# Kernel tuning notes

Hardware: AMD Instinct MI355X
Metric: run time of the kernel (lower is better)

Reference implementation:

```python
import jax, jax.numpy as jnp
import numpy as np

B, L, BERT_DIM = 8, 1024, 1024
HEADS, HEAD_SIZE = 12, 64


def setup_inputs() -> dict:
    key = jax.random.key(0)
    k1, k2, k3, k4, k5, k6 = jax.random.split(key, 6)
    s = 1.0 / np.sqrt(BERT_DIM)
    return {
        "head": jax.random.normal(k1, (B, L, BERT_DIM), dtype=jnp.float32),
        "tail": jax.random.normal(k2, (B, L, BERT_DIM), dtype=jnp.float32),
        "W_head": jax.random.normal(k3, (BERT_DIM, HEADS * HEAD_SIZE), dtype=jnp.float32) * s,
        "b_head": jax.random.normal(k4, (HEADS * HEAD_SIZE,), dtype=jnp.float32) * 0.01,
        "W_tail": jax.random.normal(k5, (BERT_DIM, HEADS * HEAD_SIZE), dtype=jnp.float32) * s,
        "b_tail": jax.random.normal(k6, (HEADS * HEAD_SIZE,), dtype=jnp.float32) * 0.01,
    }


def _sincos(seq_len, dim, dtype):
    # SinusoidalPositionEmbedding with merge_mode='zero': (L, dim), interleaved [sin, cos]
    pos = jnp.arange(seq_len, dtype=dtype)                     # (L,)
    inv = jnp.power(10000.0, -2.0 * jnp.arange(dim // 2, dtype=dtype) / dim)  # (dim/2,)
    ang = pos[:, None] * inv[None, :]                          # (L, dim/2)
    emb = jnp.stack([jnp.sin(ang), jnp.cos(ang)], axis=-1).reshape(seq_len, dim)
    # cos_pos: even/odd duplication as in torch reference
    cos_pos = jnp.repeat(emb[:, 1::2], 2, axis=-1)             # (L, dim)
    sin_pos = jnp.repeat(emb[:, 0::2], 2, axis=-1)             # (L, dim)
    return cos_pos, sin_pos


def _rotate_half(x):
    # stack([-x[...,1::2], x[...,::2]], -1).reshape(x.shape)
    return jnp.stack([-x[..., 1::2], x[..., 0::2]], axis=-1).reshape(x.shape)


def reference(head, tail, W_head, b_head, W_tail, b_tail):
    bsz, seq_len, _ = head.shape
    h = (head @ W_head + b_head).reshape(bsz, seq_len, HEADS, HEAD_SIZE)
    t = (tail @ W_tail + b_tail).reshape(bsz, seq_len, HEADS, HEAD_SIZE)

    cos_pos, sin_pos = _sincos(seq_len, HEAD_SIZE, h.dtype)
    cos_pos = cos_pos[None, :, None, :]  # (1, L, 1, D)
    sin_pos = sin_pos[None, :, None, :]

    h = h * cos_pos + _rotate_half(h) * sin_pos
    t = t * cos_pos + _rotate_half(t) * sin_pos

    # (B, H, L, L)
    logits = jnp.einsum("blhd,bmhd->bhlm", h, t)
    return logits / jnp.sqrt(jnp.asarray(HEAD_SIZE, h.dtype))
```

## Files before the change

### kernel.cpp

```cpp
#include <hip/hip_runtime.h>
#include <hip/hip_bf16.h>


#define DIM   1024
#define NOUT  768
#define NHEAD 12

typedef __attribute__((ext_vector_type(8))) short bf16x8;
typedef __attribute__((ext_vector_type(4))) float f32x4;

__device__ __forceinline__ ushort f2bf(float f) {
  union { float f; unsigned u; } v; v.f = f;
  unsigned r = v.u + 0x7fffu + ((v.u >> 16) & 1u);
  return (ushort)(r >> 16);
}

__device__ __forceinline__ void gload16(const ushort* g, ushort* l) {
  __builtin_amdgcn_global_load_lds(
      (const __attribute__((address_space(1))) unsigned int*)g,
      (__attribute__((address_space(3))) unsigned int*)l, 16, 0, 0);
}

__global__ __launch_bounds__(256) void prep_kernel(
    const float* __restrict__ head, const float* __restrict__ tail,
    const float* __restrict__ Wh,   const float* __restrict__ Wt_,
    ushort* __restrict__ Hx, ushort* __restrict__ Tx,
    ushort* __restrict__ WtH, ushort* __restrict__ WtT,
    float2* __restrict__ rope)
{
  __shared__ ushort lds[64][72];
  const int bx = blockIdx.x, tid = threadIdx.x;

  if (bx < 4096) {
    size_t t = (size_t)bx * 256 + tid;
    const float* src; ushort* dst; size_t e;
    if (t < 524288) { src = head; dst = Hx; e = t * 16; }
    else            { src = tail; dst = Tx; e = (t - 524288) * 16; }
    const float4* p = reinterpret_cast<const float4*>(src + e);
    float4 a = p[0], b = p[1], c = p[2], d = p[3];
    ushort o[16] = { f2bf(a.x), f2bf(a.y), f2bf(a.z), f2bf(a.w),
                     f2bf(b.x), f2bf(b.y), f2bf(b.z), f2bf(b.w),
                     f2bf(c.x), f2bf(c.y), f2bf(c.z), f2bf(c.w),
                     f2bf(d.x), f2bf(d.y), f2bf(d.z), f2bf(d.w) };
    *reinterpret_cast<bf16x8*>(dst + e)     = *reinterpret_cast<bf16x8*>(o);
    *reinterpret_cast<bf16x8*>(dst + e + 8) = *reinterpret_cast<bf16x8*>(o + 8);
  } else if (bx < 4480) {
    int t2 = bx - 4096;
    int wsel = t2 / 192, tile = t2 % 192;
    int k0 = (tile / 12) * 64, n0 = (tile % 12) * 64;
    const float* W = wsel ? Wt_ : Wh;
    ushort* WT = wsel ? WtT : WtH;
#pragma unroll
    for (int q = 0; q < 16; ++q) {
      int idx = q * 256 + tid;
      int kr = idx >> 6, nc = idx & 63;
      lds[nc][kr] = f2bf(W[(size_t)(k0 + kr) * NOUT + n0 + nc]);
    }
    __syncthreads();
#pragma unroll
    for (int q = 0; q < 2; ++q) {
      int idx = q * 256 + tid;
      int nc = idx >> 3, kg = idx & 7;
      *reinterpret_cast<bf16x8*>(&WT[(size_t)(n0 + nc) * DIM + k0 + kg * 8]) =
          *reinterpret_cast<bf16x8*>(&lds[nc][kg * 8]);
    }
  } else {
    int j = (bx - 4480) * 256 + tid;
    int l = j >> 5, i = j & 31;
    float inv = powf(10000.0f, -(float)i / 32.0f);
    float ang = (float)l * inv;
    rope[j] = make_float2(cosf(ang), sinf(ang));
  }
}

__global__ __launch_bounds__(256) void proj_rope_kernel(
    const ushort* __restrict__ Hx,  const ushort* __restrict__ Tx,
    const ushort* __restrict__ WtH, const ushort* __restrict__ WtT,
    const float*  __restrict__ bh,  const float*  __restrict__ bt,
    const float2* __restrict__ rope,
    ushort* __restrict__ Hb, ushort* __restrict__ Tb)
{
  const bool sel = (blockIdx.z != 0);
  const ushort* X    = sel ? Tx  : Hx;
  const ushort* Wt   = sel ? WtT : WtH;
  const float*  bias = sel ? bt  : bh;
  ushort*       Out  = sel ? Tb  : Hb;

  __shared__ ushort As[128 * 64];
  __shared__ ushort Bs[128 * 64];

  const int tid = threadIdx.x;
  const int m0 = blockIdx.x * 128;
  const int n0 = blockIdx.y * 128;
  const int wid = tid >> 6, lane = tid & 63;
  const int wm = wid >> 1, wn = wid & 1;
  const int r = lane & 15, g = lane >> 4;
  const int r7 = r & 7;

  f32x4 acc[4][4] = {};

  for (int k0 = 0; k0 < DIM; k0 += 64) {
#pragma unroll
    for (int i = 0; i < 4; ++i) {
      int task = i * 256 + tid;
      int row = task >> 3, c = task & 7;
      int csrc = c ^ (row & 7);
      gload16(X + (size_t)(m0 + row) * DIM + k0 + csrc * 8, &As[task * 8]);
    }
#pragma unroll
    for (int i = 0; i < 4; ++i) {
      int task = i * 256 + tid;
      int row = task >> 3, c = task & 7;
      int csrc = c ^ (row & 7);
      gload16(Wt + (size_t)(n0 + row) * DIM + k0 + csrc * 8, &Bs[task * 8]);
    }
    __syncthreads();

    bf16x8 af[2][4], bfv[2][4];
#pragma unroll
    for (int ks = 0; ks < 2; ++ks) {
      int cs = (ks * 4 + g) ^ r7;
#pragma unroll
      for (int m = 0; m < 4; ++m)
        af[ks][m] = *reinterpret_cast<const bf16x8*>(
            &As[(wm * 64 + m * 16 + r) * 64 + cs * 8]);
#pragma unroll
      for (int n = 0; n < 4; ++n)
        bfv[ks][n] = *reinterpret_cast<const bf16x8*>(
            &Bs[(wn * 64 + n * 16 + r) * 64 + cs * 8]);
    }
#pragma unroll
    for (int n = 0; n < 4; ++n)
#pragma unroll
      for (int m = 0; m < 4; ++m) {
        acc[n][m] = __builtin_amdgcn_mfma_f32_16x16x32_bf16(
            bfv[0][n], af[0][m], acc[n][m], 0, 0, 0);
        acc[n][m] = __builtin_amdgcn_mfma_f32_16x16x32_bf16(
            bfv[1][n], af[1][m], acc[n][m], 0, 0, 0);
      }
    __syncthreads();
  }

#pragma unroll
  for (int n = 0; n < 4; ++n) {
    int col = n0 + wn * 64 + n * 16 + g * 4;
    int hd = col >> 6, dd = col & 63;
    int ii = dd >> 1;
    float4 bs4 = *reinterpret_cast<const float4*>(&bias[col]);
#pragma unroll
    for (int m = 0; m < 4; ++m) {
      int grow = m0 + wm * 64 + m * 16 + r;
      int l = grow & 1023, b = grow >> 10;
      float4 rp = *reinterpret_cast<const float4*>(&rope[l * 32 + ii]);
      float v0 = acc[n][m][0] + bs4.x;
      float v1 = acc[n][m][1] + bs4.y;
      float v2 = acc[n][m][2] + bs4.z;
      float v3 = acc[n][m][3] + bs4.w;
      ushort o[4] = { f2bf(v0 * rp.x - v1 * rp.y),
                      f2bf(v1 * rp.x + v0 * rp.y),
                      f2bf(v2 * rp.z - v3 * rp.w),
                      f2bf(v3 * rp.z + v2 * rp.w) };
      *reinterpret_cast<ushort4*>(
          &Out[(((size_t)b * NHEAD + hd) * 1024 + l) * 64 + dd]) =
          *reinterpret_cast<ushort4*>(o);
    }
  }
}

__global__ __launch_bounds__(256) void logits_kernel(
    const ushort* __restrict__ Hb, const ushort* __restrict__ Tb,
    float* __restrict__ out)
{
  const int f = blockIdx.x;
  const int rx = f & 7, q = f >> 3;
  const int j = q & 63, zq = q >> 6;
  const int z = zq * 8 + rx;
  const int l0 = (j & 7) * 128, m0 = (j >> 3) * 128;

  const int tid = threadIdx.x;
  const int wid = tid >> 6, lane = tid & 63;
  const int wl = wid >> 1, wm = wid & 1;
  const int r = lane & 15, g = lane >> 4;
  const size_t zo = (size_t)z << 16;
  const ushort* H = Hb + zo;
  const ushort* T = Tb + zo;
  float* C = out + ((size_t)z << 20);

  bf16x8 tf[4][2], hf[4][2];
#pragma unroll
  for (int t = 0; t < 4; ++t)
#pragma unroll
    for (int ks = 0; ks < 2; ++ks) {
      tf[t][ks] = *reinterpret_cast<const bf16x8*>(
          T + (m0 + wm * 64 + t * 16 + r) * 64 + ks * 32 + g * 8);
      hf[t][ks] = *reinterpret_cast<const bf16x8*>(
          H + (l0 + wl * 64 + t * 16 + r) * 64 + ks * 32 + g * 8);
    }

  f32x4 acc[4][4] = {};
#pragma unroll
  for (int mt = 0; mt < 4; ++mt)
#pragma unroll
    for (int lt = 0; lt < 4; ++lt) {
      acc[mt][lt] = __builtin_amdgcn_mfma_f32_16x16x32_bf16(
          tf[mt][0], hf[lt][0], acc[mt][lt], 0, 0, 0);
      acc[mt][lt] = __builtin_amdgcn_mfma_f32_16x16x32_bf16(
          tf[mt][1], hf[lt][1], acc[mt][lt], 0, 0, 0);
    }

#pragma unroll
  for (int mt = 0; mt < 4; ++mt)
#pragma unroll
    for (int lt = 0; lt < 4; ++lt) {
      int l = l0 + wl * 64 + lt * 16 + r;
      int m = m0 + wm * 64 + mt * 16 + g * 4;
      f32x4 v = acc[mt][lt] * 0.125f;
      __builtin_nontemporal_store(
          v, reinterpret_cast<f32x4*>(&C[(size_t)l * 1024 + m]));
    }
}

extern "C" void kernel_launch(void* const* d_in, const int* in_sizes, int n_in,
                              void* d_out, int out_size, void* d_ws, size_t ws_size,
                              hipStream_t stream)
{
  const float* head   = (const float*)d_in[0];
  const float* tail   = (const float*)d_in[1];
  const float* W_head = (const float*)d_in[2];
  const float* b_head = (const float*)d_in[3];
  const float* W_tail = (const float*)d_in[4];
  const float* b_tail = (const float*)d_in[5];
  float* out = (float*)d_out;

  char* ws = (char*)d_ws;
  ushort* WtH  = (ushort*)(ws);
  ushort* WtT  = (ushort*)(ws + 1572864);
  float2* rope = (float2*)(ws + 3145728);
  ushort* Hb   = (ushort*)(ws + 3407872);
  ushort* Tb   = (ushort*)(ws + 15990784);

  ushort* Hx = (ushort*)d_out;
  ushort* Tx = Hx + 8388608;

  prep_kernel<<<dim3(4608), dim3(256), 0, stream>>>(
      head, tail, W_head, W_tail, Hx, Tx, WtH, WtT, rope);
  proj_rope_kernel<<<dim3(64, 6, 2), dim3(256), 0, stream>>>(
      Hx, Tx, WtH, WtT, b_head, b_tail, rope, Hb, Tb);
  logits_kernel<<<dim3(6144), dim3(256), 0, stream>>>(Hb, Tb, out);
}
```

Baseline: 173.9 us.

## Double-buffer LDS tiles in projection GEMM with K-step 32

New measurement: 193.4 us. +11.2%, slower.

```diff
diff --git a/kernel.cpp b/kernel.cpp
--- a/kernel.cpp
+++ b/kernel.cpp
@@ -86,8 +86,8 @@
   const float*  bias = sel ? bt  : bh;
   ushort*       Out  = sel ? Tb  : Hb;
 
-  __shared__ ushort As[128 * 64];
-  __shared__ ushort Bs[128 * 64];
+  __shared__ ushort As[2][128 * 32];
+  __shared__ ushort Bs[2][128 * 32];
 
   const int tid = threadIdx.x;
   const int m0 = blockIdx.x * 128;
@@ -95,51 +95,53 @@
   const int wid = tid >> 6, lane = tid & 63;
   const int wm = wid >> 1, wn = wid & 1;
   const int r = lane & 15, g = lane >> 4;
-  const int r7 = r & 7;
+
+  const int row0 = tid >> 2,         c0 = tid & 3;
+  const int row1 = (256 + tid) >> 2, c1 = tid & 3;
+  const int cs0 = c0 ^ (row0 & 3), cs1 = c1 ^ (row1 & 3);
+
+#define STAGE(buf, k0)                                                        \
+  do {                                                                        \
+    gload16(X  + (size_t)(m0 + row0) * DIM + (k0) + cs0 * 8,                  \
+            &As[buf][tid * 8]);                                               \
+    gload16(X  + (size_t)(m0 + row1) * DIM + (k0) + cs1 * 8,                  \
+            &As[buf][(256 + tid) * 8]);                                       \
+    gload16(Wt + (size_t)(n0 + row0) * DIM + (k0) + cs0 * 8,                  \
+            &Bs[buf][tid * 8]);                                               \
+    gload16(Wt + (size_t)(n0 + row1) * DIM + (k0) + cs1 * 8,                  \
+            &Bs[buf][(256 + tid) * 8]);                                       \
+  } while (0)
 
   f32x4 acc[4][4] = {};
 
-  for (int k0 = 0; k0 < DIM; k0 += 64) {
-#pragma unroll
-    for (int i = 0; i < 4; ++i) {
-      int task = i * 256 + tid;
-      int row = task >> 3, c = task & 7;
-      int csrc = c ^ (row & 7);
-      gload16(X + (size_t)(m0 + row) * DIM + k0 + csrc * 8, &As[task * 8]);
-    }
-#pragma unroll
-    for (int i = 0; i < 4; ++i) {
-      int task = i * 256 + tid;
-      int row = task >> 3, c = task & 7;
-      int csrc = c ^ (row & 7);
-      gload16(Wt + (size_t)(n0 + row) * DIM + k0 + csrc * 8, &Bs[task * 8]);
-    }
-    __syncthreads();
-
-    bf16x8 af[2][4], bfv[2][4];
-#pragma unroll
-    for (int ks = 0; ks < 2; ++ks) {
-      int cs = (ks * 4 + g) ^ r7;
+  STAGE(0, 0);
+
+  for (int t = 0; t < 32; ++t) {
+    const int cur = t & 1;
+    asm volatile("s_waitcnt vmcnt(0)" ::: "memory");
+    __builtin_amdgcn_sched_barrier(0);
+    __builtin_amdgcn_s_barrier();
+    __builtin_amdgcn_sched_barrier(0);
+    if (t < 31) STAGE(cur ^ 1, (t + 1) * 32);
+
+    bf16x8 af[4], bfv[4];
+    const int cs = g ^ (r & 3);
+#pragma unroll
+    for (int m = 0; m < 4; ++m)
+      af[m] = *reinterpret_cast<const bf16x8*>(
+          &As[cur][(wm * 64 + m * 16 + r) * 32 + cs * 8]);
+#pragma unroll
+    for (int n = 0; n < 4; ++n)
+      bfv[n] = *reinterpret_cast<const bf16x8*>(
+          &Bs[cur][(wn * 64 + n * 16 + r) * 32 + cs * 8]);
+#pragma unroll
+    for (int n = 0; n < 4; ++n)
 #pragma unroll
       for (int m = 0; m < 4; ++m)
-        af[ks][m] = *reinterpret_cast<const bf16x8*>(
-            &As[(wm * 64 + m * 16 + r) * 64 + cs * 8]);
-#pragma unroll
-      for (int n = 0; n < 4; ++n)
-        bfv[ks][n] = *reinterpret_cast<const bf16x8*>(
-            &Bs[(wn * 64 + n * 16 + r) * 64 + cs * 8]);
-    }
-#pragma unroll
-    for (int n = 0; n < 4; ++n)
-#pragma unroll
-      for (int m = 0; m < 4; ++m) {
         acc[n][m] = __builtin_amdgcn_mfma_f32_16x16x32_bf16(
-            bfv[0][n], af[0][m], acc[n][m], 0, 0, 0);
-        acc[n][m] = __builtin_amdgcn_mfma_f32_16x16x32_bf16(
-            bfv[1][n], af[1][m], acc[n][m], 0, 0, 0);
-      }
-    __syncthreads();
+            bfv[n], af[m], acc[n][m], 0, 0, 0);
   }
+#undef STAGE
 
 #pragma unroll
   for (int n = 0; n < 4; ++n) {
```
